# Kernel optimization log

Hardware: AMD Instinct MI355X
Metric: run time of the kernel (lower is better)

## Reference

```python
import jax, jax.numpy as jnp
import numpy as np

N_DOF = 7
HID = 128
BATCH = 65536
EPS_M = 1e-3      # mass-matrix PSD jitter
EPS_B = 1e-3      # friction-matrix PSD jitter
EPS_SOLVE = 1e-4  # jitter added before linalg.solve
N_CHOL = N_DOF * (N_DOF + 1) // 2  # 28
TRI_I, TRI_J = np.tril_indices(N_DOF)
DIAG_MASK = jnp.asarray(TRI_I == TRI_J)


def _mlp(x, p):
    # p = (W0,b0,W1,b1,W2,b2,W3,b3): Linear+Softplus x3 then Linear (n_layers=3)
    W0, b0, W1, b1, W2, b2, W3, b3 = p
    h = jax.nn.softplus(x @ W0 + b0)
    h = jax.nn.softplus(h @ W1 + b1)
    h = jax.nn.softplus(h @ W2 + b2)
    return h @ W3 + b3


def _psd(chol_vec, eps):
    # chol_vec: (n_chol,) lower-triangular entries row-major (i, j<=i); exp on diagonal
    vals = jnp.where(DIAG_MASK, jnp.exp(chol_vec), chol_vec)
    L = jnp.zeros((N_DOF, N_DOF), chol_vec.dtype).at[TRI_I, TRI_J].set(vals)
    return L @ L.T + eps * jnp.eye(N_DOF, dtype=chol_vec.dtype)


def _accel_single(q, qd, mp, pp, fp):
    mass = lambda qq: _psd(_mlp(qq, mp), EPS_M)

    def lagrangian(qq, qdd):
        M = mass(qq)
        V = jax.nn.softplus(_mlp(qq, pp))[0]
        return 0.5 * qdd @ (M @ qdd) - V

    dL_dq = jax.grad(lagrangian, argnums=0)(q, qd)
    # L is quadratic in qdot => Hessian wrt qdot (M_rows loop in torch) is exactly M(q)
    M = mass(q)
    # Coriolis_i = (d/dq [M(q) qd]_i) . qd  == jvp of q -> M(q) qd in direction qd
    _, coriolis = jax.jvp(lambda qq: mass(qq) @ qd, (q,), (qd,))
    B_mat = _psd(_mlp(q, fp), EPS_B)
    friction = B_mat @ qd
    rhs = dL_dq - coriolis - friction
    return jnp.linalg.solve(M + EPS_SOLVE * jnp.eye(N_DOF, dtype=q.dtype), rhs)


def setup_inputs() -> dict:
    key = jax.random.key(0)
    keys = iter(jax.random.split(key, 64))

    def lin(fan_in, fan_out):
        W = jax.random.normal(next(keys), (fan_in, fan_out), jnp.float32) / np.sqrt(fan_in)
        b = jax.random.normal(next(keys), (fan_out,), jnp.float32) * 0.01
        return W, b

    inp = {
        "q": jax.random.normal(next(keys), (BATCH, N_DOF), jnp.float32),
        "qdot": jax.random.normal(next(keys), (BATCH, N_DOF), jnp.float32),
    }
    for name, out_dim in [("m", N_CHOL), ("p", 1), ("f", N_CHOL)]:
        dims = [(N_DOF, HID), (HID, HID), (HID, HID), (HID, out_dim)]
        for li, (fi, fo) in enumerate(dims):
            W, b = lin(fi, fo)
            inp[f"{name}W{li}"] = W
            inp[f"{name}b{li}"] = b
    return inp


def reference(q, qdot,
              mW0, mb0, mW1, mb1, mW2, mb2, mW3, mb3,
              pW0, pb0, pW1, pb1, pW2, pb2, pW3, pb3,
              fW0, fb0, fW1, fb1, fW2, fb2, fW3, fb3):
    mp = (mW0, mb0, mW1, mb1, mW2, mb2, mW3, mb3)
    pp = (pW0, pb0, pW1, pb1, pW2, pb2, pW3, pb3)
    fp = (fW0, fb0, fW1, fb1, fW2, fb2, fW3, fb3)
    return jax.vmap(_accel_single, in_axes=(0, 0, None, None, None))(q, qdot, mp, pp, fp)
```

## Files before the change

### kernel.cpp

```cpp
#include <hip/hip_runtime.h>

#define NT 512
#define TM 32
#define NBLK (65536/TM)

typedef unsigned int u32;
typedef unsigned short u16;
typedef __attribute__((ext_vector_type(4))) float f32x4;
typedef __attribute__((ext_vector_type(8))) _Float16 f16x8;

namespace {
constexpr int TI_[28] = {0,1,1,2,2,2,3,3,3,3,4,4,4,4,4,5,5,5,5,5,5,6,6,6,6,6,6,6};
constexpr int TJ_[28] = {0,0,1,0,1,2,0,1,2,3,0,1,2,3,4,0,1,2,3,4,5,0,1,2,3,4,5,6};
constexpr bool DG_[28] = {1,0,1,0,0,1,0,0,0,1,0,0,0,0,1,0,0,0,0,0,1,0,0,0,0,0,0,1};

constexpr int IB[20] = {0,16384,81920,147456,163840,180224,245760,311296,319488,
                        335872,401408,466944,475136,540672,606208,614400,630784,
                        696320,761856,778240};
constexpr int IN_[19]  = {128,128,128,32,128,128,128,16,128,128,128,16,128,128,16,128,128,128,32};
constexpr int ITY_[19] = {0,1,1,2,3,4,4,5,0,1,1,6,4,4,5,0,1,1,2};
constexpr int TOTF16 = 778240/2;
}

__device__ __forceinline__ float sp_f(float z) {
  float t = exp2f(-fabsf(z)*1.44269504f);
  return fmaxf(z, 0.f) + 0.69314718f*__log2f(1.f + t);
}
__device__ __forceinline__ float sigm_f(float z) {
  float t = exp2f(-z*1.44269504f);
  return __builtin_amdgcn_rcpf(1.f + t);
}
__device__ __forceinline__ float sig_a(float a) {
  return 1.f - exp2f(-a*1.44269504f);
}

__device__ __forceinline__ u16 h2b(_Float16 h) { union{_Float16 f; u16 u;} c; c.f = h; return c.u; }
__device__ __forceinline__ u16 f16b(float x)   { return h2b((_Float16)x); }
__device__ __forceinline__ float b2f(u16 b)    { union{u16 u; _Float16 f;} c; c.u = b; return (float)c.f; }
__device__ __forceinline__ f16x8 fz8()         { return (f16x8)(_Float16)0.f; }

__device__ __forceinline__ f32x4 mm(f16x8 a, f16x8 b, f32x4 c) {
  return __builtin_amdgcn_mfma_f32_16x16x32_f16(a, b, c, 0, 0, 0);
}

__device__ __forceinline__ f16x8 aread(const u16* P, int row, int s) {
  return *(const f16x8*)(P + row*128 + ((s ^ (row & 7)) << 3));
}
__device__ __forceinline__ void awrite(u16* P, int m, int n, u16 v) {
  P[m*128 + (((n >> 3) ^ (m & 7)) << 3) + (n & 7)] = v;
}
__device__ __forceinline__ float sread(const u16* P, int m, int n) {
  return b2f(P[m*128 + (((n >> 3) ^ (m & 7)) << 3) + (n & 7)]);
}
__device__ __forceinline__ f16x8 aq8(const u16* P, int row, int lq) {
  f16x8 v = *(const f16x8*)(P + row*8);
  return lq ? fz8() : v;
}
__device__ __forceinline__ f16x8 ubread(const u16* P, int row, int lq) {
  return *(const f16x8*)(P + row*32 + ((lq ^ (row & 3)) << 3));
}
__device__ __forceinline__ f16x8 bread(const char* img, int N, int sk, int n) {
  return *(const f16x8*)(img + ((sk*N + n) << 4));
}
__device__ __forceinline__ float ctread(const float* cT, int u, int m) {
  return cT[u*32 + (((m >> 2) ^ (u & 7)) << 2) + (m & 3)];
}
__device__ __forceinline__ void ctwrite(float* cT, int u, int m, float v) {
  cT[u*32 + (((m >> 2) ^ (u & 7)) << 2) + (m & 3)] = v;
}

struct __align__(16) Smem {
  u16 mh1[4096], mh2[4096], mh3[4096];
  u16 gA[4096], gB[4096];
  u16 pH1[4096], pH2[4096], pH3[4096];
  u16 qmh[256], qml[256], qdb[256];
  u16 ub[1024];
  float cTm[896];
  u16 dcH[896], cfH[896];
  float GQ1[384], GQp[384];
  float V[32];
};
static_assert(sizeof(Smem) <= 81920, "need 2 blocks/CU");

template<int KS, bool QSRC>
__device__ __forceinline__ void fwd_hl(const u16* Ah, const u16* Al, u16* Oh, u16* Ol,
                                       const char* img, int hb, const float* bias,
                                       int wg, int l) {
  const int lr = l & 15, lq = l >> 4;
  f32x4 H[2][2], X[2][2];
  #pragma unroll
  for (int j=0;j<2;++j)
    #pragma unroll
    for (int mt=0;mt<2;++mt) { H[j][mt]=(f32x4){0,0,0,0}; X[j][mt]=(f32x4){0,0,0,0}; }
  #pragma unroll
  for (int ks=0; ks<KS; ++ks) {
    const int sk = ks*4 + lq;
    f16x8 ah[2], al[2];
    #pragma unroll
    for (int mt=0;mt<2;++mt) {
      const int row = mt*16+lr;
      ah[mt] = QSRC ? aq8(Ah,row,lq) : aread(Ah,row,sk);
      al[mt] = QSRC ? aq8(Al,row,lq) : aread(Al,row,sk);
    }
    #pragma unroll
    for (int j=0;j<2;++j) {
      const int n = (wg + j*4)*16 + lr;
      const f16x8 bh = bread(img,128,sk,n);
      const f16x8 bl = bread(img+hb,128,sk,n);
      #pragma unroll
      for (int mt=0;mt<2;++mt) {
        H[j][mt]=mm(ah[mt],bh,H[j][mt]);
        X[j][mt]=mm(ah[mt],bl,X[j][mt]);
        X[j][mt]=mm(al[mt],bh,X[j][mt]);
      }
    }
  }
  #pragma unroll
  for (int j=0;j<2;++j) {
    const int n = (wg + j*4)*16 + lr;
    const float bv = bias ? bias[n] : 0.f;
    #pragma unroll
    for (int mt=0;mt<2;++mt)
      #pragma unroll
      for (int r=0;r<4;++r) {
        const int m = mt*16 + lq*4 + r;
        const float o = sp_f(H[j][mt][r] + X[j][mt][r]*(1.f/4096.f) + bv);
        const _Float16 hh = (_Float16)o;
        awrite(Oh, m, n, h2b(hh));
        awrite(Ol, m, n, f16b((o - (float)hh)*4096.f));
      }
  }
}

template<int KS, bool QSRC, int TC>
__device__ __forceinline__ void fwd_h(const u16* Ah, u16* Oh, const char* img,
                                      const float* bias, int tile0, int tstep, int l) {
  const int lr = l & 15, lq = l >> 4;
  f32x4 H[TC][2];
  #pragma unroll
  for (int j=0;j<TC;++j)
    #pragma unroll
    for (int mt=0;mt<2;++mt) H[j][mt]=(f32x4){0,0,0,0};
  #pragma unroll
  for (int ks=0; ks<KS; ++ks) {
    const int sk = ks*4 + lq;
    f16x8 ah[2];
    #pragma unroll
    for (int mt=0;mt<2;++mt) {
      const int row = mt*16+lr;
      ah[mt] = QSRC ? aq8(Ah,row,lq) : aread(Ah,row,sk);
    }
    #pragma unroll
    for (int j=0;j<TC;++j) {
      const int n = (tile0 + j*tstep)*16 + lr;
      const f16x8 bh = bread(img,128,sk,n);
      #pragma unroll
      for (int mt=0;mt<2;++mt) H[j][mt]=mm(ah[mt],bh,H[j][mt]);
    }
  }
  #pragma unroll
  for (int j=0;j<TC;++j) {
    const int n = (tile0 + j*tstep)*16 + lr;
    const float bv = bias ? bias[n] : 0.f;
    #pragma unroll
    for (int mt=0;mt<2;++mt)
      #pragma unroll
      for (int r=0;r<4;++r) {
        const int m = mt*16 + lq*4 + r;
        awrite(Oh, m, n, f16b(sp_f(H[j][mt][r] + bv)));
      }
  }
}

__device__ __forceinline__ void grad128(const u16* Ain, const u16* Sig, u16* Out,
                                        const char* img, int wg, int l) {
  const int lr = l & 15, lq = l >> 4;
  f32x4 acc[2][2];
  #pragma unroll
  for (int j=0;j<2;++j)
    #pragma unroll
    for (int mt=0;mt<2;++mt) acc[j][mt]=(f32x4){0,0,0,0};
  #pragma unroll
  for (int ks=0; ks<4; ++ks) {
    const int sk = ks*4 + lq;
    f16x8 ah[2];
    #pragma unroll
    for (int mt=0;mt<2;++mt) ah[mt] = aread(Ain, mt*16+lr, sk);
    #pragma unroll
    for (int j=0;j<2;++j) {
      const int n = (wg + j*4)*16 + lr;
      const f16x8 bh = bread(img,128,sk,n);
      #pragma unroll
      for (int mt=0;mt<2;++mt) acc[j][mt]=mm(ah[mt],bh,acc[j][mt]);
    }
  }
  #pragma unroll
  for (int j=0;j<2;++j) {
    const int n = (wg + j*4)*16 + lr;
    #pragma unroll
    for (int mt=0;mt<2;++mt)
      #pragma unroll
      for (int r=0;r<4;++r) {
        const int m = mt*16 + lq*4 + r;
        const float s = sig_a(sread(Sig, m, n));
        awrite(Out, m, n, f16b(s * acc[j][mt][r]));
      }
  }
}

template<int ASRC>
__device__ __forceinline__ void grad32(const u16* Ain, const u16* Sig, u16* Out,
                                       const char* img, int wg, int l) {
  const int lr = l & 15, lq = l >> 4;
  f32x4 acc[2][2];
  #pragma unroll
  for (int j=0;j<2;++j)
    #pragma unroll
    for (int mt=0;mt<2;++mt) acc[j][mt]=(f32x4){0,0,0,0};
  {
    f16x8 ah[2];
    #pragma unroll
    for (int mt=0;mt<2;++mt) {
      const int row = mt*16+lr;
      ah[mt] = (ASRC==0) ? ubread(Ain,row,lq) : aq8(Ain,row,lq);
    }
    #pragma unroll
    for (int j=0;j<2;++j) {
      const int n = (wg + j*4)*16 + lr;
      const f16x8 bh = bread(img,128,lq,n);
      #pragma unroll
      for (int mt=0;mt<2;++mt) acc[j][mt]=mm(ah[mt],bh,acc[j][mt]);
    }
  }
  #pragma unroll
  for (int j=0;j<2;++j) {
    const int n = (wg + j*4)*16 + lr;
    #pragma unroll
    for (int mt=0;mt<2;++mt)
      #pragma unroll
      for (int r=0;r<4;++r) {
        const int m = mt*16 + lq*4 + r;
        const float s = sig_a(sread(Sig, m, n));
        awrite(Out, m, n, f16b(s * acc[j][mt][r]));
      }
  }
}

__device__ __forceinline__ void gradPotF(const u16* A3p, const float* V, float pb3v,
                                         const u16* Sig, u16* Out, const char* img,
                                         int wg, int l) {
  const int lr = l & 15, lq = l >> 4;
  float up[2];
  #pragma unroll
  for (int mt=0;mt<2;++mt) up[mt] = sigm_f(V[mt*16+lr] + pb3v);
  f32x4 acc[2][2];
  #pragma unroll
  for (int j=0;j<2;++j)
    #pragma unroll
    for (int mt=0;mt<2;++mt) acc[j][mt]=(f32x4){0,0,0,0};
  #pragma unroll
  for (int ks=0; ks<4; ++ks) {
    const int sk = ks*4 + lq;
    f16x8 af[2];
    #pragma unroll
    for (int mt=0;mt<2;++mt) {
      const f16x8 a3 = aread(A3p, mt*16+lr, sk);
      f16x8 t;
      #pragma unroll
      for (int e=0;e<8;++e) t[e] = (_Float16)(up[mt]*sig_a((float)a3[e]));
      af[mt] = t;
    }
    #pragma unroll
    for (int j=0;j<2;++j) {
      const int n = (wg + j*4)*16 + lr;
      const f16x8 bh = bread(img,128,sk,n);
      #pragma unroll
      for (int mt=0;mt<2;++mt) acc[j][mt]=mm(af[mt],bh,acc[j][mt]);
    }
  }
  #pragma unroll
  for (int j=0;j<2;++j) {
    const int n = (wg + j*4)*16 + lr;
    #pragma unroll
    for (int mt=0;mt<2;++mt)
      #pragma unroll
      for (int r=0;r<4;++r) {
        const int m = mt*16 + lq*4 + r;
        const float s = sig_a(sread(Sig, m, n));
        awrite(Out, m, n, f16b(s * acc[j][mt][r]));
      }
  }
}

template<bool HL>
__device__ __forceinline__ void l3(const u16* Ah, const u16* Al, const char* img, int hb,
                                   const float* b3, float* cT, u16* cH, int wg, int l) {
  const int lr = l & 15, lq = l >> 4;
  const int mt = wg & 1, ntl = wg >> 1;
  const int n = ntl*16 + lr;
  f32x4 H = {0,0,0,0}, X = {0,0,0,0};
  #pragma unroll
  for (int ks=0; ks<4; ++ks) {
    const int sk = ks*4 + lq;
    const int row = mt*16+lr;
    const f16x8 bh = bread(img,32,sk,n);
    const f16x8 ah = aread(Ah,row,sk);
    H = mm(ah,bh,H);
    if (HL) {
      const f16x8 bl = bread(img+hb,32,sk,n);
      const f16x8 al = aread(Al,row,sk);
      X = mm(ah,bl,X);
      X = mm(al,bh,X);
    }
  }
  if (n < 28) {
    const float bv = b3 ? b3[n] : 0.f;
    if (HL) {
      f32x4 v;
      #pragma unroll
      for (int r=0;r<4;++r) v[r] = H[r] + X[r]*(1.f/4096.f) + bv;
      const int m0 = mt*16 + lq*4;
      *(f32x4*)&cT[n*32 + (((m0 >> 2) ^ (n & 7)) << 2)] = v;
    } else {
      #pragma unroll
      for (int r=0;r<4;++r) cH[n*32 + mt*16 + lq*4 + r] = f16b(H[r] + bv);
    }
  }
}

template<bool HEAD>
__device__ __forceinline__ void n16(const u16* Ain, const char* img,
                                    float* GQ, float* V, int g, int l) {
  const int lr = l & 15, lq = l >> 4;
  f32x4 acc = {0,0,0,0};
  #pragma unroll
  for (int ks=0; ks<4; ++ks) {
    const int sk = ks*4 + lq;
    const f16x8 bh = bread(img,16,sk,lr);
    const f16x8 ah = aread(Ain, g*16+lr, sk);
    acc = mm(ah,bh,acc);
  }
  #pragma unroll
  for (int r=0;r<4;++r) {
    const int m = g*16 + lq*4 + r;
    if (HEAD) { if (lr == 0) V[m] = acc[r]; }
    else      { if (lr < 8)  GQ[m*12 + lr] = acc[r]; }
  }
}

__global__ __launch_bounds__(256)
void pack_kernel(const float* __restrict__ mW0, const float* __restrict__ mb0,
                 const float* __restrict__ mW1, const float* __restrict__ mW2,
                 const float* __restrict__ mW3,
                 const float* __restrict__ pW0, const float* __restrict__ pb0,
                 const float* __restrict__ pW1, const float* __restrict__ pW2,
                 const float* __restrict__ pW3,
                 const float* __restrict__ fW0, const float* __restrict__ fb0,
                 const float* __restrict__ fW1, const float* __restrict__ fW2,
                 const float* __restrict__ fW3,
                 u16* __restrict__ ws)
{
  const int idx = blockIdx.x*256 + threadIdx.x;
  if (idx >= TOTF16) return;
  int img = 0;
  #pragma unroll
  for (int i = 1; i < 19; ++i) if (idx >= IB[i]/2) img = i;
  const int rem = idx - IB[img]/2;
  const int N = IN_[img];
  const int psz = (IB[img+1] - IB[img]) / 4;
  const int plane = rem >= psz;
  const int e = plane ? rem - psz : rem;
  const int slot = e / (N*8);
  const int r1 = e - slot*(N*8);
  const int n = r1 >> 3, ee = r1 & 7;
  const int k = slot*8 + ee;

  const float* W = nullptr; const float* B = nullptr;
  switch (img) {
    case 0:  W = mW0; B = mb0; break;
    case 1:  W = mW1; break;   case 2:  W = mW2; break;
    case 3:  W = mW3; break;   case 4:  W = mW3; break;
    case 5:  W = mW2; break;   case 6:  W = mW1; break;
    case 7:  W = mW0; break;
    case 8:  W = pW0; B = pb0; break;
    case 9:  W = pW1; break;   case 10: W = pW2; break;
    case 11: W = pW3; break;   case 12: W = pW2; break;
    case 13: W = pW1; break;   case 14: W = pW0; break;
    case 15: W = fW0; B = fb0; break;
    case 16: W = fW1; break;   case 17: W = fW2; break;
    default: W = fW3; break;
  }
  float v = 0.f;
  switch (ITY_[img]) {
    case 0: v = (k < 7) ? W[k*128 + n] : (k == 7 ? B[n] : 0.f); break;
    case 1: v = W[k*128 + n]; break;
    case 2: v = (n < 28) ? W[k*28 + n] : 0.f; break;
    case 3: v = (k < 28) ? W[n*28 + k] : 0.f; break;
    case 4: v = W[n*128 + k]; break;
    case 5: v = (n < 7) ? W[n*128 + k] : 0.f; break;
    default: v = (n == 0) ? W[k] : 0.f; break;
  }
  if (img == 12) v *= pW3[k];
  const _Float16 h = (_Float16)v;
  union { _Float16 f; u16 u; } c;
  c.f = plane ? (_Float16)((v - (float)h) * 4096.f) : h;
  ws[idx] = c.u;
}

__global__ __launch_bounds__(NT, 4)
void delan_kernel(const float* __restrict__ qg, const float* __restrict__ qdg,
    const float* __restrict__ mb1, const float* __restrict__ mb2, const float* __restrict__ mb3,
    const float* __restrict__ pb1, const float* __restrict__ pb2, const float* __restrict__ pb3,
    const float* __restrict__ fb1, const float* __restrict__ fb2, const float* __restrict__ fb3,
    const char* __restrict__ ws, float* __restrict__ out)
{
  __shared__ Smem S;
  const int t = threadIdx.x;
  const int l = t & 63;
  const int w = __builtin_amdgcn_readfirstlane(t >> 6);
  const int wg = w & 3;
  const int s0 = blockIdx.x * TM;

  if (t < 256) {
    const int m = t >> 3, c = t & 7;
    const float v = (c < 7) ? qg[(s0 + m)*7 + c] : 1.f;
    const _Float16 hh = (_Float16)v;
    S.qmh[t] = h2b(hh);
    S.qml[t] = f16b((v - (float)hh)*4096.f);
  } else {
    const int idx = t - 256;
    const int m = idx >> 3, c = idx & 7;
    S.qdb[idx] = (c < 7) ? f16b(qdg[(s0 + m)*7 + c]) : (u16)0;
  }
  __syncthreads();

  if (w < 4) fwd_hl<1,true>(S.qmh,S.qml,S.mh1,S.gA, ws+IB[0],(IB[1]-IB[0])/2, nullptr, wg, l);
  else       fwd_h<1,true,2>(S.qmh, S.pH1, ws+IB[8], nullptr, wg, 4, l);
  __syncthreads();
  if (w < 4) fwd_hl<4,false>(S.mh1,S.gA,S.mh2,S.gB, ws+IB[1],(IB[2]-IB[1])/2, mb1, wg, l);
  else       fwd_h<4,false,2>(S.pH1, S.pH2, ws+IB[9], pb1, wg, 4, l);
  __syncthreads();
  if (w < 4) fwd_hl<4,false>(S.mh2,S.gB,S.mh3,S.gA, ws+IB[2],(IB[3]-IB[2])/2, mb2, wg, l);
  else       fwd_h<4,false,2>(S.pH2, S.pH3, ws+IB[10], pb2, wg, 4, l);
  __syncthreads();
  if (w < 4)      l3<true>(S.mh3, S.gA, ws+IB[3],(IB[4]-IB[3])/2, mb3, S.cTm, nullptr, wg, l);
  else if (w < 6) n16<true>(S.pH3, ws+IB[11], nullptr, S.V, w-4, l);
  __syncthreads();
  if (w == 0 && l < 32) {
    const int ml = l;
    float qdv[7];
    #pragma unroll
    for (int i = 0; i < 7; ++i) qdv[i] = qdg[(s0 + ml)*7 + i];
    float vals[28], wvv[7] = {0,0,0,0,0,0,0};
    #pragma unroll
    for (int u = 0; u < 28; ++u) {
      const float cv = ctread(S.cTm, u, ml);
      vals[u] = DG_[u] ? __expf(cv) : cv;
    }
    #pragma unroll
    for (int u = 0; u < 28; ++u) wvv[TJ_[u]] = fmaf(vals[u], qdv[TI_[u]], wvv[TJ_[u]]);
    #pragma unroll
    for (int u = 0; u < 28; ++u) ctwrite(S.cTm, u, ml, vals[u]);
    #pragma unroll
    for (int u = 0; u < 28; ++u) {
      const float uval = (DG_[u] ? vals[u] : 1.f) * qdv[TI_[u]] * wvv[TJ_[u]];
      S.ub[ml*32 + (((u >> 3) ^ (ml & 3)) << 3) + (u & 7)] = f16b(uval);
    }
    #pragma unroll
    for (int u = 28; u < 32; ++u)
      S.ub[ml*32 + (((u >> 3) ^ (ml & 3)) << 3) + (u & 7)] = 0;
  } else if (w >= 4) {
    gradPotF(S.pH3, S.V, pb3[0], S.pH2, S.pH2, ws+IB[12], wg, l);
  }
  __syncthreads();
  if (w < 4) grad32<0>(S.ub, S.mh3, S.gB, ws+IB[4], wg, l);
  else       grad128(S.pH2, S.pH1, S.pH1, ws+IB[13], wg, l);
  __syncthreads();
  if (w < 4)      grad128(S.gB, S.mh2, S.gA, ws+IB[5], wg, l);
  else if (w < 6) n16<false>(S.pH1, ws+IB[14], S.GQp, nullptr, w-4, l);
  __syncthreads();
  if (w < 4) grad128(S.gA, S.mh1, S.gB, ws+IB[6], wg, l);
  else       grad32<1>(S.qdb, S.mh1, S.pH2, ws+IB[0], wg, l);
  __syncthreads();
  if (w < 2)      n16<false>(S.gB, ws+IB[7], S.GQ1, nullptr, w, l);
  else if (w < 4) fwd_h<1,true,4>(S.qmh, S.gA, ws+IB[15], nullptr, w-2, 2, l);
  else            grad128(S.pH2, S.mh2, S.pH3, ws+IB[1], wg, l);
  __syncthreads();
  if (w < 4) fwd_h<4,false,2>(S.gA, S.gB, ws+IB[16], fb1, wg, 4, l);
  else       grad128(S.pH3, S.mh3, S.pH2, ws+IB[2], wg, l);
  __syncthreads();
  if (w < 4) fwd_h<4,false,2>(S.gB, S.gA, ws+IB[17], fb2, wg, 4, l);
  else       l3<false>(S.pH2, nullptr, ws+IB[3], 0, nullptr, nullptr, S.dcH, wg, l);
  __syncthreads();
  if (w < 4) l3<false>(S.gA, nullptr, ws+IB[18], 0, fb3, nullptr, S.cfH, wg, l);
  __syncthreads();

  if (w == 0 && l < 32) {
    const int ml = l;
    float qdv[7];
    #pragma unroll
    for (int i = 0; i < 7; ++i) qdv[i] = qdg[(s0 + ml)*7 + i];
    float lv[28];
    #pragma unroll
    for (int u = 0; u < 28; ++u) lv[u] = ctread(S.cTm, u, ml);
    float wvv[7] = {0,0,0,0,0,0,0};
    #pragma unroll
    for (int u = 0; u < 28; ++u) wvv[TJ_[u]] = fmaf(lv[u], qdv[TI_[u]], wvv[TJ_[u]]);
    float cor[7] = {0,0,0,0,0,0,0}, t2[7] = {0,0,0,0,0,0,0};
    #pragma unroll
    for (int u = 0; u < 28; ++u) {
      const float dv = (DG_[u] ? lv[u] : 1.f) * b2f(S.dcH[u*32 + ml]);
      cor[TI_[u]] = fmaf(dv, wvv[TJ_[u]], cor[TI_[u]]);
      t2[TJ_[u]]  = fmaf(dv, qdv[TI_[u]], t2[TJ_[u]]);
    }
    #pragma unroll
    for (int u = 0; u < 28; ++u) cor[TI_[u]] = fmaf(lv[u], t2[TJ_[u]], cor[TI_[u]]);
    float r7[7];
    #pragma unroll
    for (int i = 0; i < 7; ++i)
      r7[i] = S.GQ1[ml*12 + i] - cor[i] - S.GQp[ml*12 + i] - 1e-3f*qdv[i];
    float fv[28];
    #pragma unroll
    for (int u = 0; u < 28; ++u) {
      const float cv = b2f(S.cfH[u*32 + ml]);
      fv[u] = DG_[u] ? __expf(cv) : cv;
    }
    float wf[7] = {0,0,0,0,0,0,0};
    #pragma unroll
    for (int u = 0; u < 28; ++u) wf[TJ_[u]] = fmaf(fv[u], qdv[TI_[u]], wf[TJ_[u]]);
    #pragma unroll
    for (int u = 0; u < 28; ++u) r7[TI_[u]] -= fv[u]*wf[TJ_[u]];

    float L[7][7];
    #pragma unroll
    for (int i = 0; i < 7; ++i)
      #pragma unroll
      for (int j = 0; j < 7; ++j) L[i][j] = 0.f;
    #pragma unroll
    for (int u = 0; u < 28; ++u) L[TI_[u]][TJ_[u]] = lv[u];

    float M[7][7];
    #pragma unroll
    for (int i = 0; i < 7; ++i)
      #pragma unroll
      for (int j = 0; j < 7; ++j)
        if (j <= i) {
          float sum = (i == j) ? 1.1e-3f : 0.f;
          #pragma unroll
          for (int k = 0; k < 7; ++k) if (k <= j) sum = fmaf(L[i][k], L[j][k], sum);
          M[i][j] = sum;
        }
    float C[7][7];
    #pragma unroll
    for (int i = 0; i < 7; ++i)
      #pragma unroll
      for (int j = 0; j < 7; ++j)
        if (j <= i) {
          float sum = M[i][j];
          #pragma unroll
          for (int k = 0; k < 7; ++k) if (k < j) sum -= C[i][k] * C[j][k];
          if (j == i) C[i][j] = sqrtf(fmaxf(sum, 1e-12f));
          else        C[i][j] = sum / C[j][j];
        }
    float y[7];
    #pragma unroll
    for (int i = 0; i < 7; ++i) {
      float sum = r7[i];
      #pragma unroll
      for (int k = 0; k < 7; ++k) if (k < i) sum -= C[i][k] * y[k];
      y[i] = sum / C[i][i];
    }
    float x[7];
    #pragma unroll
    for (int i = 6; i >= 0; --i) {
      float sum = y[i];
      #pragma unroll
      for (int k = 0; k < 7; ++k) if (k > i) sum -= C[k][i] * x[k];
      x[i] = sum / C[i][i];
    }
    #pragma unroll
    for (int i = 0; i < 7; ++i) out[(s0 + ml)*7 + i] = x[i];
  }
}

extern "C" void kernel_launch(void* const* d_in, const int* in_sizes, int n_in,
                              void* d_out, int out_size, void* d_ws, size_t ws_size,
                              hipStream_t stream) {
  (void)in_sizes; (void)n_in; (void)out_size; (void)ws_size;
  const float* q   = (const float*)d_in[0];
  const float* qd  = (const float*)d_in[1];
  const float* mW0 = (const float*)d_in[2];  const float* mb0 = (const float*)d_in[3];
  const float* mW1 = (const float*)d_in[4];  const float* mb1 = (const float*)d_in[5];
  const float* mW2 = (const float*)d_in[6];  const float* mb2 = (const float*)d_in[7];
  const float* mW3 = (const float*)d_in[8];  const float* mb3 = (const float*)d_in[9];
  const float* pW0 = (const float*)d_in[10]; const float* pb0 = (const float*)d_in[11];
  const float* pW1 = (const float*)d_in[12]; const float* pb1 = (const float*)d_in[13];
  const float* pW2 = (const float*)d_in[14]; const float* pb2 = (const float*)d_in[15];
  const float* pW3 = (const float*)d_in[16]; const float* pb3 = (const float*)d_in[17];
  const float* fW0 = (const float*)d_in[18]; const float* fb0 = (const float*)d_in[19];
  const float* fW1 = (const float*)d_in[20]; const float* fb1 = (const float*)d_in[21];
  const float* fW2 = (const float*)d_in[22]; const float* fb2 = (const float*)d_in[23];
  const float* fW3 = (const float*)d_in[24]; const float* fb3 = (const float*)d_in[25];
  float* out = (float*)d_out;
  u16* ws = (u16*)d_ws;

  pack_kernel<<<dim3((TOTF16 + 255)/256), dim3(256), 0, stream>>>(
      mW0, mb0, mW1, mW2, mW3, pW0, pb0, pW1, pW2, pW3, fW0, fb0, fW1, fW2, fW3, ws);

  delan_kernel<<<dim3(NBLK), dim3(NT), 0, stream>>>(
      q, qd, mb1, mb2, mb3, pb1, pb2, pb3, fb1, fb2, fb3,
      (const char*)ws, out);
}
```

Baseline: 133.6 us.

## Swap MFMA operand roles so epilogues write contiguous 4-wide fp16 vectors

Every MFMA now takes the weights as the A operand and the activations as the B operand. Each lane's four accumulator values then lie along the feature dimension for one batch row, so the epilogues can load the sigmoid inputs and the bias as vectors and store four fp16 outputs at once instead of making scalar swizzled LDS accesses. The cTm layout drops its swizzle and the per-sample scalar code indexes it directly. The aim is fewer LDS instructions and less address arithmetic in the epilogues, at the risk of bank conflicts on the now unswizzled cTm accesses.

```diff
diff --git a/kernel.cpp b/kernel.cpp
--- a/kernel.cpp
+++ b/kernel.cpp
@@ -8,6 +8,7 @@
 typedef unsigned short u16;
 typedef __attribute__((ext_vector_type(4))) float f32x4;
 typedef __attribute__((ext_vector_type(8))) _Float16 f16x8;
+typedef __attribute__((ext_vector_type(4))) _Float16 f16x4;
 
 namespace {
 constexpr int TI_[28] = {0,1,1,2,2,2,3,3,3,3,4,4,4,4,4,5,5,5,5,5,5,6,6,6,6,6,6,6};
@@ -46,27 +47,24 @@
 __device__ __forceinline__ f16x8 aread(const u16* P, int row, int s) {
   return *(const f16x8*)(P + row*128 + ((s ^ (row & 7)) << 3));
 }
-__device__ __forceinline__ void awrite(u16* P, int m, int n, u16 v) {
-  P[m*128 + (((n >> 3) ^ (m & 7)) << 3) + (n & 7)] = v;
-}
-__device__ __forceinline__ float sread(const u16* P, int m, int n) {
-  return b2f(P[m*128 + (((n >> 3) ^ (m & 7)) << 3) + (n & 7)]);
-}
-__device__ __forceinline__ f16x8 aq8(const u16* P, int row, int lq) {
+__device__ __forceinline__ int aidx4(int mrow, int n2) {
+  return mrow*128 + (((n2 >> 3) ^ (mrow & 7)) << 3) + (n2 & 7);
+}
+__device__ __forceinline__ void awrite4(u16* P, int mrow, int n2, f16x4 v) {
+  *(f16x4*)(P + aidx4(mrow, n2)) = v;
+}
+__device__ __forceinline__ f16x4 aread4(const u16* P, int mrow, int n2) {
+  return *(const f16x4*)(P + aidx4(mrow, n2));
+}
+__device__ __forceinline__ f16x8 aq8(const u16* P, int row, int g) {
   f16x8 v = *(const f16x8*)(P + row*8);
-  return lq ? fz8() : v;
-}
-__device__ __forceinline__ f16x8 ubread(const u16* P, int row, int lq) {
-  return *(const f16x8*)(P + row*32 + ((lq ^ (row & 3)) << 3));
+  return g ? fz8() : v;
+}
+__device__ __forceinline__ f16x8 ubread(const u16* P, int row, int g) {
+  return *(const f16x8*)(P + row*32 + ((g ^ (row & 3)) << 3));
 }
 __device__ __forceinline__ f16x8 bread(const char* img, int N, int sk, int n) {
   return *(const f16x8*)(img + ((sk*N + n) << 4));
-}
-__device__ __forceinline__ float ctread(const float* cT, int u, int m) {
-  return cT[u*32 + (((m >> 2) ^ (u & 7)) << 2) + (m & 3)];
-}
-__device__ __forceinline__ void ctwrite(float* cT, int u, int m, float v) {
-  cT[u*32 + (((m >> 2) ^ (u & 7)) << 2) + (m & 3)] = v;
 }
 
 struct __align__(16) Smem {
@@ -83,10 +81,10 @@
 static_assert(sizeof(Smem) <= 81920, "need 2 blocks/CU");
 
 template<int KS, bool QSRC>
-__device__ __forceinline__ void fwd_hl(const u16* Ah, const u16* Al, u16* Oh, u16* Ol,
+__device__ __forceinline__ void fwd_hl(const u16* Bh, const u16* Bl, u16* Oh, u16* Ol,
                                        const char* img, int hb, const float* bias,
                                        int wg, int l) {
-  const int lr = l & 15, lq = l >> 4;
+  const int m = l & 15, g = l >> 4;
   f32x4 H[2][2], X[2][2];
   #pragma unroll
   for (int j=0;j<2;++j)
@@ -94,48 +92,52 @@
     for (int mt=0;mt<2;++mt) { H[j][mt]=(f32x4){0,0,0,0}; X[j][mt]=(f32x4){0,0,0,0}; }
   #pragma unroll
   for (int ks=0; ks<KS; ++ks) {
-    const int sk = ks*4 + lq;
-    f16x8 ah[2], al[2];
-    #pragma unroll
-    for (int mt=0;mt<2;++mt) {
-      const int row = mt*16+lr;
-      ah[mt] = QSRC ? aq8(Ah,row,lq) : aread(Ah,row,sk);
-      al[mt] = QSRC ? aq8(Al,row,lq) : aread(Al,row,sk);
+    const int sk = ks*4 + g;
+    f16x8 bh[2], bl[2];
+    #pragma unroll
+    for (int mt=0;mt<2;++mt) {
+      const int row = mt*16+m;
+      bh[mt] = QSRC ? aq8(Bh,row,g) : aread(Bh,row,sk);
+      bl[mt] = QSRC ? aq8(Bl,row,g) : aread(Bl,row,sk);
     }
     #pragma unroll
     for (int j=0;j<2;++j) {
-      const int n = (wg + j*4)*16 + lr;
-      const f16x8 bh = bread(img,128,sk,n);
-      const f16x8 bl = bread(img+hb,128,sk,n);
+      const int n2t = wg + j*4;
+      const f16x8 wh = bread(img,128,sk, n2t*16+m);
+      const f16x8 wl = bread(img+hb,128,sk, n2t*16+m);
       #pragma unroll
       for (int mt=0;mt<2;++mt) {
-        H[j][mt]=mm(ah[mt],bh,H[j][mt]);
-        X[j][mt]=mm(ah[mt],bl,X[j][mt]);
-        X[j][mt]=mm(al[mt],bh,X[j][mt]);
+        H[j][mt]=mm(wh,bh[mt],H[j][mt]);
+        X[j][mt]=mm(wl,bh[mt],X[j][mt]);
+        X[j][mt]=mm(wh,bl[mt],X[j][mt]);
       }
     }
   }
   #pragma unroll
   for (int j=0;j<2;++j) {
-    const int n = (wg + j*4)*16 + lr;
-    const float bv = bias ? bias[n] : 0.f;
-    #pragma unroll
-    for (int mt=0;mt<2;++mt)
+    const int n2 = (wg + j*4)*16 + 4*g;
+    f32x4 bv = bias ? *(const f32x4*)(bias + n2) : (f32x4){0,0,0,0};
+    #pragma unroll
+    for (int mt=0;mt<2;++mt) {
+      const int mrow = mt*16 + m;
+      f16x4 vh, vl;
       #pragma unroll
       for (int r=0;r<4;++r) {
-        const int m = mt*16 + lq*4 + r;
-        const float o = sp_f(H[j][mt][r] + X[j][mt][r]*(1.f/4096.f) + bv);
+        const float o = sp_f(H[j][mt][r] + X[j][mt][r]*(1.f/4096.f) + bv[r]);
         const _Float16 hh = (_Float16)o;
-        awrite(Oh, m, n, h2b(hh));
-        awrite(Ol, m, n, f16b((o - (float)hh)*4096.f));
+        vh[r] = hh;
+        vl[r] = (_Float16)((o - (float)hh)*4096.f);
       }
+      awrite4(Oh, mrow, n2, vh);
+      awrite4(Ol, mrow, n2, vl);
+    }
   }
 }
 
 template<int KS, bool QSRC, int TC>
-__device__ __forceinline__ void fwd_h(const u16* Ah, u16* Oh, const char* img,
+__device__ __forceinline__ void fwd_h(const u16* Bh, u16* Oh, const char* img,
                                       const float* bias, int tile0, int tstep, int l) {
-  const int lr = l & 15, lq = l >> 4;
+  const int m = l & 15, g = l >> 4;
   f32x4 H[TC][2];
   #pragma unroll
   for (int j=0;j<TC;++j)
@@ -143,38 +145,38 @@
     for (int mt=0;mt<2;++mt) H[j][mt]=(f32x4){0,0,0,0};
   #pragma unroll
   for (int ks=0; ks<KS; ++ks) {
-    const int sk = ks*4 + lq;
-    f16x8 ah[2];
-    #pragma unroll
-    for (int mt=0;mt<2;++mt) {
-      const int row = mt*16+lr;
-      ah[mt] = QSRC ? aq8(Ah,row,lq) : aread(Ah,row,sk);
+    const int sk = ks*4 + g;
+    f16x8 bh[2];
+    #pragma unroll
+    for (int mt=0;mt<2;++mt) {
+      const int row = mt*16+m;
+      bh[mt] = QSRC ? aq8(Bh,row,g) : aread(Bh,row,sk);
     }
     #pragma unroll
     for (int j=0;j<TC;++j) {
-      const int n = (tile0 + j*tstep)*16 + lr;
-      const f16x8 bh = bread(img,128,sk,n);
-      #pragma unroll
-      for (int mt=0;mt<2;++mt) H[j][mt]=mm(ah[mt],bh,H[j][mt]);
+      const f16x8 wh = bread(img,128,sk,(tile0 + j*tstep)*16+m);
+      #pragma unroll
+      for (int mt=0;mt<2;++mt) H[j][mt]=mm(wh,bh[mt],H[j][mt]);
     }
   }
   #pragma unroll
   for (int j=0;j<TC;++j) {
-    const int n = (tile0 + j*tstep)*16 + lr;
-    const float bv = bias ? bias[n] : 0.f;
-    #pragma unroll
-    for (int mt=0;mt<2;++mt)
-      #pragma unroll
-      for (int r=0;r<4;++r) {
-        const int m = mt*16 + lq*4 + r;
-        awrite(Oh, m, n, f16b(sp_f(H[j][mt][r] + bv)));
-      }
-  }
-}
-
-__device__ __forceinline__ void grad128(const u16* Ain, const u16* Sig, u16* Out,
+    const int n2 = (tile0 + j*tstep)*16 + 4*g;
+    f32x4 bv = bias ? *(const f32x4*)(bias + n2) : (f32x4){0,0,0,0};
+    #pragma unroll
+    for (int mt=0;mt<2;++mt) {
+      const int mrow = mt*16 + m;
+      f16x4 vh;
+      #pragma unroll
+      for (int r=0;r<4;++r) vh[r] = (_Float16)sp_f(H[j][mt][r] + bv[r]);
+      awrite4(Oh, mrow, n2, vh);
+    }
+  }
+}
+
+__device__ __forceinline__ void grad128(const u16* Bin, const u16* Sig, u16* Out,
                                         const char* img, int wg, int l) {
-  const int lr = l & 15, lq = l >> 4;
+  const int m = l & 15, g = l >> 4;
   f32x4 acc[2][2];
   #pragma unroll
   for (int j=0;j<2;++j)
@@ -182,77 +184,77 @@
     for (int mt=0;mt<2;++mt) acc[j][mt]=(f32x4){0,0,0,0};
   #pragma unroll
   for (int ks=0; ks<4; ++ks) {
-    const int sk = ks*4 + lq;
-    f16x8 ah[2];
-    #pragma unroll
-    for (int mt=0;mt<2;++mt) ah[mt] = aread(Ain, mt*16+lr, sk);
+    const int sk = ks*4 + g;
+    f16x8 bh[2];
+    #pragma unroll
+    for (int mt=0;mt<2;++mt) bh[mt] = aread(Bin, mt*16+m, sk);
     #pragma unroll
     for (int j=0;j<2;++j) {
-      const int n = (wg + j*4)*16 + lr;
-      const f16x8 bh = bread(img,128,sk,n);
-      #pragma unroll
-      for (int mt=0;mt<2;++mt) acc[j][mt]=mm(ah[mt],bh,acc[j][mt]);
+      const f16x8 wh = bread(img,128,sk,(wg + j*4)*16+m);
+      #pragma unroll
+      for (int mt=0;mt<2;++mt) acc[j][mt]=mm(wh,bh[mt],acc[j][mt]);
     }
   }
   #pragma unroll
   for (int j=0;j<2;++j) {
-    const int n = (wg + j*4)*16 + lr;
-    #pragma unroll
-    for (int mt=0;mt<2;++mt)
-      #pragma unroll
-      for (int r=0;r<4;++r) {
-        const int m = mt*16 + lq*4 + r;
-        const float s = sig_a(sread(Sig, m, n));
-        awrite(Out, m, n, f16b(s * acc[j][mt][r]));
-      }
+    const int n2 = (wg + j*4)*16 + 4*g;
+    #pragma unroll
+    for (int mt=0;mt<2;++mt) {
+      const int mrow = mt*16 + m;
+      const f16x4 sg = aread4(Sig, mrow, n2);
+      f16x4 o;
+      #pragma unroll
+      for (int r=0;r<4;++r) o[r] = (_Float16)(sig_a((float)sg[r]) * acc[j][mt][r]);
+      awrite4(Out, mrow, n2, o);
+    }
   }
 }
 
 template<int ASRC>
-__device__ __forceinline__ void grad32(const u16* Ain, const u16* Sig, u16* Out,
+__device__ __forceinline__ void grad32(const u16* Bin, const u16* Sig, u16* Out,
                                        const char* img, int wg, int l) {
-  const int lr = l & 15, lq = l >> 4;
+  const int m = l & 15, g = l >> 4;
   f32x4 acc[2][2];
   #pragma unroll
   for (int j=0;j<2;++j)
     #pragma unroll
     for (int mt=0;mt<2;++mt) acc[j][mt]=(f32x4){0,0,0,0};
   {
-    f16x8 ah[2];
-    #pragma unroll
-    for (int mt=0;mt<2;++mt) {
-      const int row = mt*16+lr;
-      ah[mt] = (ASRC==0) ? ubread(Ain,row,lq) : aq8(Ain,row,lq);
+    f16x8 bh[2];
+    #pragma unroll
+    for (int mt=0;mt<2;++mt) {
+      const int row = mt*16+m;
+      bh[mt] = (ASRC==0) ? ubread(Bin,row,g) : aq8(Bin,row,g);
     }
     #pragma unroll
     for (int j=0;j<2;++j) {
-      const int n = (wg + j*4)*16 + lr;
-      const f16x8 bh = bread(img,128,lq,n);
-      #pragma unroll
-      for (int mt=0;mt<2;++mt) acc[j][mt]=mm(ah[mt],bh,acc[j][mt]);
+      const f16x8 wh = bread(img,128,g,(wg + j*4)*16+m);
+      #pragma unroll
+      for (int mt=0;mt<2;++mt) acc[j][mt]=mm(wh,bh[mt],acc[j][mt]);
     }
   }
   #pragma unroll
   for (int j=0;j<2;++j) {
-    const int n = (wg + j*4)*16 + lr;
-    #pragma unroll
-    for (int mt=0;mt<2;++mt)
-      #pragma unroll
-      for (int r=0;r<4;++r) {
-        const int m = mt*16 + lq*4 + r;
-        const float s = sig_a(sread(Sig, m, n));
-        awrite(Out, m, n, f16b(s * acc[j][mt][r]));
-      }
+    const int n2 = (wg + j*4)*16 + 4*g;
+    #pragma unroll
+    for (int mt=0;mt<2;++mt) {
+      const int mrow = mt*16 + m;
+      const f16x4 sg = aread4(Sig, mrow, n2);
+      f16x4 o;
+      #pragma unroll
+      for (int r=0;r<4;++r) o[r] = (_Float16)(sig_a((float)sg[r]) * acc[j][mt][r]);
+      awrite4(Out, mrow, n2, o);
+    }
   }
 }
 
 __device__ __forceinline__ void gradPotF(const u16* A3p, const float* V, float pb3v,
                                          const u16* Sig, u16* Out, const char* img,
                                          int wg, int l) {
-  const int lr = l & 15, lq = l >> 4;
+  const int m = l & 15, g = l >> 4;
   float up[2];
   #pragma unroll
-  for (int mt=0;mt<2;++mt) up[mt] = sigm_f(V[mt*16+lr] + pb3v);
+  for (int mt=0;mt<2;++mt) up[mt] = sigm_f(V[mt*16+m] + pb3v);
   f32x4 acc[2][2];
   #pragma unroll
   for (int j=0;j<2;++j)
@@ -260,91 +262,90 @@
     for (int mt=0;mt<2;++mt) acc[j][mt]=(f32x4){0,0,0,0};
   #pragma unroll
   for (int ks=0; ks<4; ++ks) {
-    const int sk = ks*4 + lq;
-    f16x8 af[2];
-    #pragma unroll
-    for (int mt=0;mt<2;++mt) {
-      const f16x8 a3 = aread(A3p, mt*16+lr, sk);
+    const int sk = ks*4 + g;
+    f16x8 bh[2];
+    #pragma unroll
+    for (int mt=0;mt<2;++mt) {
+      const f16x8 a3 = aread(A3p, mt*16+m, sk);
       f16x8 t;
       #pragma unroll
       for (int e=0;e<8;++e) t[e] = (_Float16)(up[mt]*sig_a((float)a3[e]));
-      af[mt] = t;
+      bh[mt] = t;
     }
     #pragma unroll
     for (int j=0;j<2;++j) {
-      const int n = (wg + j*4)*16 + lr;
-      const f16x8 bh = bread(img,128,sk,n);
-      #pragma unroll
-      for (int mt=0;mt<2;++mt) acc[j][mt]=mm(af[mt],bh,acc[j][mt]);
+      const f16x8 wh = bread(img,128,sk,(wg + j*4)*16+m);
+      #pragma unroll
+      for (int mt=0;mt<2;++mt) acc[j][mt]=mm(wh,bh[mt],acc[j][mt]);
     }
   }
   #pragma unroll
   for (int j=0;j<2;++j) {
-    const int n = (wg + j*4)*16 + lr;
-    #pragma unroll
-    for (int mt=0;mt<2;++mt)
-      #pragma unroll
-      for (int r=0;r<4;++r) {
-        const int m = mt*16 + lq*4 + r;
-        const float s = sig_a(sread(Sig, m, n));
-        awrite(Out, m, n, f16b(s * acc[j][mt][r]));
-      }
+    const int n2 = (wg + j*4)*16 + 4*g;
+    #pragma unroll
+    for (int mt=0;mt<2;++mt) {
+      const int mrow = mt*16 + m;
+      const f16x4 sg = aread4(Sig, mrow, n2);
+      f16x4 o;
+      #pragma unroll
+      for (int r=0;r<4;++r) o[r] = (_Float16)(sig_a((float)sg[r]) * acc[j][mt][r]);
+      awrite4(Out, mrow, n2, o);
+    }
   }
 }
 
 template<bool HL>
-__device__ __forceinline__ void l3(const u16* Ah, const u16* Al, const char* img, int hb,
+__device__ __forceinline__ void l3(const u16* Bh, const u16* Bl, const char* img, int hb,
                                    const float* b3, float* cT, u16* cH, int wg, int l) {
-  const int lr = l & 15, lq = l >> 4;
-  const int mt = wg & 1, ntl = wg >> 1;
-  const int n = ntl*16 + lr;
+  const int m = l & 15, g = l >> 4;
+  const int n2t = wg & 1, mt = wg >> 1;
+  const int mrow = mt*16 + m;
   f32x4 H = {0,0,0,0}, X = {0,0,0,0};
   #pragma unroll
   for (int ks=0; ks<4; ++ks) {
-    const int sk = ks*4 + lq;
-    const int row = mt*16+lr;
-    const f16x8 bh = bread(img,32,sk,n);
-    const f16x8 ah = aread(Ah,row,sk);
-    H = mm(ah,bh,H);
+    const int sk = ks*4 + g;
+    const f16x8 bh = aread(Bh, mrow, sk);
+    const f16x8 wh = bread(img,32,sk, n2t*16+m);
+    H = mm(wh, bh, H);
     if (HL) {
-      const f16x8 bl = bread(img+hb,32,sk,n);
-      const f16x8 al = aread(Al,row,sk);
-      X = mm(ah,bl,X);
-      X = mm(al,bh,X);
-    }
-  }
-  if (n < 28) {
-    const float bv = b3 ? b3[n] : 0.f;
-    if (HL) {
-      f32x4 v;
-      #pragma unroll
-      for (int r=0;r<4;++r) v[r] = H[r] + X[r]*(1.f/4096.f) + bv;
-      const int m0 = mt*16 + lq*4;
-      *(f32x4*)&cT[n*32 + (((m0 >> 2) ^ (n & 7)) << 2)] = v;
-    } else {
-      #pragma unroll
-      for (int r=0;r<4;++r) cH[n*32 + mt*16 + lq*4 + r] = f16b(H[r] + bv);
+      const f16x8 wl = bread(img+hb,32,sk, n2t*16+m);
+      const f16x8 bl = aread(Bl, mrow, sk);
+      X = mm(wl, bh, X);
+      X = mm(wh, bl, X);
+    }
+  }
+  const int u0 = n2t*16 + 4*g;
+  if (u0 < 28) {
+    f32x4 bv = b3 ? *(const f32x4*)(b3 + u0) : (f32x4){0,0,0,0};
+    #pragma unroll
+    for (int r=0;r<4;++r) {
+      const float v = H[r] + (HL ? X[r]*(1.f/4096.f) : 0.f) + bv[r];
+      if (HL) cT[(u0+r)*32 + mrow] = v;
+      else    cH[(u0+r)*32 + mrow] = f16b(v);
     }
   }
 }
 
 template<bool HEAD>
-__device__ __forceinline__ void n16(const u16* Ain, const char* img,
-                                    float* GQ, float* V, int g, int l) {
-  const int lr = l & 15, lq = l >> 4;
+__device__ __forceinline__ void n16(const u16* Bin, const char* img,
+                                    float* GQ, float* V, int mt, int l) {
+  const int m = l & 15, g = l >> 4;
+  const int mrow = mt*16 + m;
   f32x4 acc = {0,0,0,0};
   #pragma unroll
   for (int ks=0; ks<4; ++ks) {
-    const int sk = ks*4 + lq;
-    const f16x8 bh = bread(img,16,sk,lr);
-    const f16x8 ah = aread(Ain, g*16+lr, sk);
-    acc = mm(ah,bh,acc);
-  }
-  #pragma unroll
-  for (int r=0;r<4;++r) {
-    const int m = g*16 + lq*4 + r;
-    if (HEAD) { if (lr == 0) V[m] = acc[r]; }
-    else      { if (lr < 8)  GQ[m*12 + lr] = acc[r]; }
+    const int sk = ks*4 + g;
+    const f16x8 bh = aread(Bin, mrow, sk);
+    const f16x8 wh = bread(img,16,sk,m);
+    acc = mm(wh, bh, acc);
+  }
+  if (HEAD) {
+    if (g == 0) V[mrow] = acc[0];
+  } else {
+    if (g < 2) {
+      #pragma unroll
+      for (int r=0;r<4;++r) GQ[mrow*12 + 4*g + r] = acc[r];
+    }
   }
 }
 
@@ -454,13 +455,13 @@
     float vals[28], wvv[7] = {0,0,0,0,0,0,0};
     #pragma unroll
     for (int u = 0; u < 28; ++u) {
-      const float cv = ctread(S.cTm, u, ml);
+      const float cv = S.cTm[u*32 + ml];
       vals[u] = DG_[u] ? __expf(cv) : cv;
     }
     #pragma unroll
     for (int u = 0; u < 28; ++u) wvv[TJ_[u]] = fmaf(vals[u], qdv[TI_[u]], wvv[TJ_[u]]);
     #pragma unroll
-    for (int u = 0; u < 28; ++u) ctwrite(S.cTm, u, ml, vals[u]);
+    for (int u = 0; u < 28; ++u) S.cTm[u*32 + ml] = vals[u];
     #pragma unroll
     for (int u = 0; u < 28; ++u) {
       const float uval = (DG_[u] ? vals[u] : 1.f) * qdv[TI_[u]] * wvv[TJ_[u]];
@@ -502,7 +503,7 @@
     for (int i = 0; i < 7; ++i) qdv[i] = qdg[(s0 + ml)*7 + i];
     float lv[28];
     #pragma unroll
-    for (int u = 0; u < 28; ++u) lv[u] = ctread(S.cTm, u, ml);
+    for (int u = 0; u < 28; ++u) lv[u] = S.cTm[u*32 + ml];
     float wvv[7] = {0,0,0,0,0,0,0};
     #pragma unroll
     for (int u = 0; u < 28; ++u) wvv[TJ_[u]] = fmaf(lv[u], qdv[TI_[u]], wvv[TJ_[u]]);
```

New measurement: 117.2 us. 12.3% less time.
